# Performance work log

Measured on AMD Instinct MI355X. Metric: run time of the kernel, lower is better.

The kernel has to match this reference:

```python
import jax, jax.numpy as jnp
import numpy as np

DIM = 256
HID = int(DIM * 2.66)        # 680
CH = 2 * HID                 # 1360, TVConv channels
K = 3
K2 = K * K
HP, WP = 14, 14
POSI = 4
INTER = min(64, HID // 2)    # 64
EPS = 1e-5


def conv2d(x, w, pad):
    # x: (B, Cin, H, W), w: (Cout, Cin, kh, kw)
    return jax.lax.conv_general_dilated(
        x, w, window_strides=(1, 1), padding=[(pad, pad), (pad, pad)],
        dimension_numbers=("NCHW", "OIHW", "NCHW"))


def layernorm_chw(x, g, b):
    # torch nn.LayerNorm([C, H, W]): normalize over last 3 dims, affine (C,H,W)
    mu = jnp.mean(x, axis=(1, 2, 3), keepdims=True)
    var = jnp.var(x, axis=(1, 2, 3), keepdims=True)
    return (x - mu) * jax.lax.rsqrt(var + EPS) * g + b


def weight_layers(posi_map, w0, g0, b0, w1, g1, b1, w2, g2, b2, wf):
    h = jax.nn.relu(layernorm_chw(conv2d(posi_map, w0, 1), g0, b0))
    h = jax.nn.relu(layernorm_chw(conv2d(h, w1, 1), g1, b1))
    h = jax.nn.relu(layernorm_chw(conv2d(h, w2, 1), g2, b2))
    return conv2d(h, wf, 1)  # (1, CH*K2, HP, WP)


def tvconv(x, weight):
    # x: (B, CH, HP, WP); weight: (1, CH, K2, HP, WP)
    B, C, H, W = x.shape
    xp = jnp.pad(x, ((0, 0), (0, 0), (1, 1), (1, 1)))
    # unfold ordering: channel-major, kernel positions row-major -> axis=2
    patches = jnp.stack([xp[:, :, i:i + H, j:j + W]
                         for i in range(K) for j in range(K)], axis=2)
    return jnp.sum(weight * patches, axis=2)  # (B, CH, H, W)


def frfn_forward(x, W_in, posi_map, w0, g0, b0, w1, g1, b1, w2, g2, b2, wf, W_out):
    h = jnp.einsum('oc,bchw->bohw', W_in, x)                      # project_in (1x1)
    wgt = weight_layers(posi_map, w0, g0, b0, w1, g1, b1, w2, g2, b2, wf)
    wgt = wgt.reshape(1, CH, K2, HP, WP)
    h = tvconv(h, wgt)                                            # (B, CH, H, W)
    x1, x2 = h[:, :HID], h[:, HID:]
    h = jax.nn.gelu(x1, approximate=False) * x2
    return jnp.einsum('oc,bchw->bohw', W_out, h)                  # project_out (1x1)


def setup_inputs() -> dict:
    key = jax.random.key(0)
    ks = jax.random.split(key, 16)
    s = 0.02
    out_chans = CH * K2
    return {
        "x": jax.random.normal(ks[0], (64, DIM, HP, WP), jnp.float32),
        "W_in": jax.random.normal(ks[1], (CH, DIM), jnp.float32) * s,
        "posi_map": jnp.ones((1, POSI, HP, WP), jnp.float32),
        "w0": jax.random.normal(ks[2], (INTER, POSI, K, K), jnp.float32) * s,
        "g0": jnp.ones((INTER, HP, WP), jnp.float32),
        "b0": jnp.zeros((INTER, HP, WP), jnp.float32),
        "w1": jax.random.normal(ks[3], (INTER, INTER, K, K), jnp.float32) * s,
        "g1": jnp.ones((INTER, HP, WP), jnp.float32),
        "b1": jnp.zeros((INTER, HP, WP), jnp.float32),
        "w2": jax.random.normal(ks[4], (INTER, INTER, K, K), jnp.float32) * s,
        "g2": jnp.ones((INTER, HP, WP), jnp.float32),
        "b2": jnp.zeros((INTER, HP, WP), jnp.float32),
        "wf": jax.random.normal(ks[5], (out_chans, INTER, K, K), jnp.float32) * s,
        "W_out": jax.random.normal(ks[6], (DIM, HID), jnp.float32) * s,
    }


def reference(x, W_in, posi_map, w0, g0, b0, w1, g1, b1, w2, g2, b2, wf, W_out):
    return frfn_forward(x, W_in, posi_map, w0, g0, b0, w1, g1, b1, w2, g2, b2, wf, W_out)
```

## Files before the change

kernel.cpp:

```cpp
#include <hip/hip_runtime.h>
#include <math.h>

#define DIMC   256
#define HID    680
#define CHN    1360
#define HP     14
#define WP     14
#define P      196
#define POSI   4
#define INTER  64
#define BATCH  64
#define KPAD   704
#define OUTCH  12240
#define MW     1408
#define MTOT   12672
#define KIM    576
#define MPADIN 1408
#define EPSLN  1e-5f

typedef __attribute__((ext_vector_type(8))) short short8;
typedef __attribute__((ext_vector_type(4))) short short4v;
typedef __attribute__((ext_vector_type(4))) float f32x4;

#define OFS_WBIN  0u
#define OFS_WBOUT 720896u
#define OFS_XT    1081344u
#define OFS_V0    7503872u
#define OFS_V1    7554048u
#define OFS_V2    7604224u
#define OFS_WGTT  7654656u
#define OFS_H1T   12452736u
#define OFS_HGT   46580608u
#define OFS_IMC   64242560u
#define OFS_WFB   64468352u
#define OFS_PST   79066496u

__device__ __forceinline__ unsigned short f2bf(float f) {
    union { float f; unsigned u; } v; v.f = f;
    unsigned u = v.u;
    return (unsigned short)((u + 0x7FFFu + ((u >> 16) & 1u)) >> 16);
}
__device__ __forceinline__ float bf2f(unsigned short h) {
    union { unsigned u; float f; } v; v.u = ((unsigned)h) << 16; return v.f;
}

__device__ __forceinline__ void gl2lds16(const unsigned short* g, unsigned short* l) {
    __builtin_amdgcn_global_load_lds(
        (const __attribute__((address_space(1))) unsigned int*)g,
        (__attribute__((address_space(3))) unsigned int*)l, 16, 0, 0);
}
__device__ __forceinline__ short8 fragld64(const unsigned short* S, int row, int lp) {
    int slot = ((row >> 1) + lp) & 7;
    return *(const short8*)(S + row * 64 + slot * 8);
}

__device__ __forceinline__ void block_reduce2(float& s, float& ss, float* red, int tid, int nthreads) {
    #pragma unroll
    for (int off = 32; off > 0; off >>= 1) {
        s  += __shfl_down(s, off);
        ss += __shfl_down(ss, off);
    }
    int wid = tid >> 6, nw = nthreads >> 6;
    if ((tid & 63) == 0) { red[wid*2] = s; red[wid*2+1] = ss; }
    __syncthreads();
    if (tid == 0) {
        float S = 0.f, SS = 0.f;
        for (int i = 0; i < nw; i++) { S += red[i*2]; SS += red[i*2+1]; }
        red[0] = S; red[1] = SS;
    }
    __syncthreads();
    s = red[0]; ss = red[1];
}

__device__ __forceinline__ void sum_pstat(const float* __restrict__ pstat, int base,
                                          float& s, float& ss) {
    s = 0.f; ss = 0.f;
    #pragma unroll
    for (int i = 0; i < 49; i++) {
        s  += pstat[base + 2*i];
        ss += pstat[base + 2*i + 1];
    }
}

#define NWIN  (MPADIN*DIMC)
#define NWOUT (DIMC*KPAD)
#define XT0   49
#define WF0   561
#define C0    2343
#define IMZ0  2475
#define PRE_BLKS 2489

__global__ __launch_bounds__(256) void k_pre(const float* __restrict__ Win,
                                             const float* __restrict__ Wout,
                                             const float* __restrict__ x,
                                             const float* __restrict__ wf,
                                             const float* __restrict__ posi,
                                             const float* __restrict__ w0,
                                             unsigned short* __restrict__ Wbin,
                                             unsigned short* __restrict__ Wbout,
                                             unsigned short* __restrict__ Xt,
                                             unsigned short* __restrict__ wfb,
                                             unsigned short* __restrict__ imc,
                                             float* __restrict__ v0,
                                             float* __restrict__ pstat) {
    __shared__ __align__(16) float smem[6304];
    int bid = blockIdx.x, tid = threadIdx.x;
    if (bid < XT0) {
        float (*ppad)[16][16] = (float(*)[16][16])smem;
        float* red = smem + 1024;
        for (int i = tid; i < POSI * 256; i += 256) {
            int cc = i >> 8, r = i & 255, ly = r >> 4, lx = r & 15;
            float v = 0.f;
            if (ly >= 1 && ly <= HP && lx >= 1 && lx <= WP) v = posi[cc*P + (ly-1)*WP + (lx-1)];
            ppad[cc][ly][lx] = v;
        }
        __syncthreads();
        int gid = bid * 256 + tid;
        int c = gid / P, p = gid - c*P, y = p / WP, x2 = p - (p/WP)*WP;
        float v = 0.f;
        #pragma unroll
        for (int ci = 0; ci < POSI; ci++) {
            const float* wr = w0 + (c*POSI + ci)*9;
            v += wr[0]*ppad[ci][y  ][x2] + wr[1]*ppad[ci][y  ][x2+1] + wr[2]*ppad[ci][y  ][x2+2]
               + wr[3]*ppad[ci][y+1][x2] + wr[4]*ppad[ci][y+1][x2+1] + wr[5]*ppad[ci][y+1][x2+2]
               + wr[6]*ppad[ci][y+2][x2] + wr[7]*ppad[ci][y+2][x2+1] + wr[8]*ppad[ci][y+2][x2+2];
        }
        v0[gid] = v;
        float s = v, ss = v * v;
        block_reduce2(s, ss, red, tid, 256);
        if (tid == 0) { pstat[2*bid] = s; pstat[2*bid + 1] = ss; }
    } else if (bid < WF0) {
        int b2 = bid - XT0;
        int b = b2 >> 3, c0 = (b2 & 7) * 32;
        float* xs = smem;
        for (int i = tid; i < 32 * 49; i += 256) {
            int ci = i / 49, p4 = (i - ci * 49) * 4;
            float4 v = *(const float4*)(x + ((size_t)b * DIMC + c0 + ci) * P + p4);
            float* d = xs + ci * 197 + p4;
            d[0] = v.x; d[1] = v.y; d[2] = v.z; d[3] = v.w;
        }
        __syncthreads();
        for (int j = tid; j < P * 4; j += 256) {
            int pp = j >> 2, c8 = (j & 3) * 8;
            short8 o;
            #pragma unroll
            for (int e = 0; e < 8; e++) o[e] = (short)f2bf(xs[(c8 + e) * 197 + pp]);
            *(short8*)(Xt + ((size_t)b * P + pp) * DIMC + c0 + c8) = o;
        }
    } else if (bid < C0) {
        int base = (bid - WF0) * 1024;
        #pragma unroll
        for (int k2 = 0; k2 < 4; k2++) {
            int t = base + k2 * 256 + tid;
            int j = t * 4;
            int rowi = j / KIM, q = j - rowi * KIM;
            int kk = rowi / MW, ch = rowi - kk * MW;
            short4v sv = (short4v)0;
            if (ch < CHN) {
                float4 v = *(const float4*)(wf + ((size_t)(ch * 9 + kk)) * KIM + q);
                sv[0] = (short)f2bf(v.x); sv[1] = (short)f2bf(v.y);
                sv[2] = (short)f2bf(v.z); sv[3] = (short)f2bf(v.w);
            }
            *(short4v*)(wfb + j) = sv;
        }
    } else if (bid < IMZ0) {
        int base = (bid - C0) * 1024;
        #pragma unroll
        for (int k2 = 0; k2 < 4; k2++) {
            int t = base + k2 * 256 + tid;
            int i0 = t * 4;
            if (i0 < NWIN) {
                short4v sv = (short4v)0;
                if (i0 < CHN * DIMC) {
                    float4 v = *(const float4*)(Win + i0);
                    sv[0] = (short)f2bf(v.x); sv[1] = (short)f2bf(v.y);
                    sv[2] = (short)f2bf(v.z); sv[3] = (short)f2bf(v.w);
                }
                *(short4v*)(Wbin + i0) = sv;
            } else {
                int j0 = i0 - NWIN;
                int o = j0 / KPAD, k = j0 - o * KPAD;
                short4v sv = (short4v)0;
                if (k < HID) {
                    float4 v = *(const float4*)(Wout + o * HID + k);
                    sv[0] = (short)f2bf(v.x); sv[1] = (short)f2bf(v.y);
                    sv[2] = (short)f2bf(v.z); sv[3] = (short)f2bf(v.w);
                }
                *(short4v*)(Wbout + j0) = sv;
            }
        }
    } else {
        int base = (bid - IMZ0) * 1024;
        #pragma unroll
        for (int k2 = 0; k2 < 4; k2++) {
            int cc = base + k2 * 256 + tid;
            if (cc < (P * KIM) / 8) *(short8*)(imc + cc * 8) = (short8)0;
        }
    }
}


__device__ __forceinline__ void dev_convln(char* sm, int bid, int tid,
                                           const float* __restrict__ v_in,
                                           const float* __restrict__ g,
                                           const float* __restrict__ b,
                                           const float* __restrict__ w,
                                           float* __restrict__ v_out,
                                           float* __restrict__ pstat,
                                           int psi, int pso) {
    float* asf = (float*)sm;
    float* wlf = asf + INTER * 256;
    float* red = wlf + 3 * INTER * 12;
    const float inv = 1.f / (float)(INTER * P);
    float s0, ss0;
    sum_pstat(pstat, psi, s0, ss0);
    float mu = s0 * inv;
    float var = ss0 * inv - mu * mu;
    float rstd = rsqrtf(var + EPSLN);

    int gid0 = bid * 256;
    int cA = gid0 / P;
    for (int i = tid; i < 3 * INTER * 9; i += 512) {
        int cc = i / (INTER * 9), rest = i - cc * (INTER * 9);
        int ci = rest / 9, kk = rest - ci * 9;
        int crow = cA + cc; if (crow >= INTER) crow = INTER - 1;
        wlf[cc * (INTER * 12) + ci * 12 + kk] = w[(crow * INTER + ci) * 9 + kk];
    }
    for (int i = tid; i < INTER * 64; i += 512)
        *(f32x4*)(asf + i * 4) = (f32x4)0.f;
    __syncthreads();
    #pragma unroll
    for (int it = 0; it < 7; it++) {
        int q4 = it * 512 + tid;
        if (q4 < (INTER * P) / 4) {
            float4 vv = *(const float4*)(v_in + q4 * 4);
            float4 gg = *(const float4*)(g + q4 * 4);
            float4 bb = *(const float4*)(b + q4 * 4);
            float va[4] = {vv.x, vv.y, vv.z, vv.w};
            float ga[4] = {gg.x, gg.y, gg.z, gg.w};
            float ba[4] = {bb.x, bb.y, bb.z, bb.w};
            #pragma unroll
            for (int e = 0; e < 4; e++) {
                int idx = q4 * 4 + e;
                int ci = idx / P, p = idx - ci * P;
                int yy = p / WP, xx = p - yy * WP;
                float a = (va[e] - mu) * rstd * ga[e] + ba[e];
                asf[ci * 256 + (yy + 1) * 16 + (xx + 1)] = a > 0.f ? a : 0.f;
            }
        }
    }
    __syncthreads();
    float s = 0.f, ss = 0.f;
    if (tid < 256) {
        int gid = gid0 + tid;
        int c = gid / P, p = gid - c * P, y = p / WP, x = p - (p / WP) * WP;
        const float* wr0 = wlf + (c - cA) * (INTER * 12);
        float v = 0.f;
        for (int ci = 0; ci < INTER; ci++) {
            const float* wi = wr0 + ci * 12;
            const float* a0 = asf + ci * 256 + y * 16 + x;
            v += wi[0]*a0[0]  + wi[1]*a0[1]  + wi[2]*a0[2]
               + wi[3]*a0[16] + wi[4]*a0[17] + wi[5]*a0[18]
               + wi[6]*a0[32] + wi[7]*a0[33] + wi[8]*a0[34];
        }
        v_out[gid] = v;
        s = v; ss = v * v;
    }
    block_reduce2(s, ss, red, tid, 512);
    if (tid == 0) { pstat[pso + 2*bid] = s; pstat[pso + 2*bid + 1] = ss; }
}

__device__ __forceinline__ void dev_lnsc(int bid, int tid,
                                         const float* __restrict__ v_in,
                                         const float* __restrict__ g,
                                         const float* __restrict__ b,
                                         const float* __restrict__ pstat,
                                         unsigned short* __restrict__ imc) {
    if (tid >= 256) return;
    const float inv = 1.f / (float)(INTER * P);
    int gid = bid * 256 + tid;
    float s0, ss0;
    sum_pstat(pstat, 196, s0, ss0);
    float mu = s0 * inv;
    float var = ss0 * inv - mu * mu;
    float rstd = rsqrtf(var + EPSLN);
    float a = (v_in[gid] - mu) * rstd * g[gid] + b[gid];
    a = a > 0.f ? a : 0.f;
    unsigned short bv = f2bf(a);
    int ci = gid / P, p = gid - ci * P, y = p / WP, x = p - (p / WP) * WP;
    #pragma unroll
    for (int k = 0; k < 9; k++) {
        int yp = y - (k / 3 - 1), xp = x - (k % 3 - 1);
        if (yp >= 0 && yp < HP && xp >= 0 && xp < WP)
            imc[(yp * WP + xp) * KIM + ci * 9 + k] = bv;
    }
}

#define GIN_MT 11
#define GIN_NT 49
#define GIN_BLKS (GIN_MT * GIN_NT)
__device__ __forceinline__ void dev_gemm_in(char* sm, int mb, int nb, int tid,
                                            const unsigned short* __restrict__ A,
                                            const unsigned short* __restrict__ B,
                                            unsigned short* __restrict__ C) {
    unsigned short* As = (unsigned short*)sm;
    unsigned short* Bs = As + 128 * 64;
    int w = tid >> 6, lane = tid & 63, quad = lane >> 4, c16 = lane & 15;
    int m0 = mb * 128, n0 = nb * 256;
    int wm = (w & 1) * 64, wn = (w >> 1) * 64;
    f32x4 acc[4][4];
    #pragma unroll
    for (int i = 0; i < 4; i++)
        #pragma unroll
        for (int j = 0; j < 4; j++) acc[i][j] = (f32x4)0.f;

    for (int kc = 0; kc < 4; ++kc) {
        int k0 = kc * 64;
        if (kc) __syncthreads();
        #pragma unroll
        for (int i = tid; i < 1024; i += 512) {
            int r = i >> 3, s = i & 7, q = (s - (r >> 1)) & 7;
            gl2lds16(A + (size_t)(m0 + r) * DIMC + k0 + q * 8, As + (i & ~63) * 8);
        }
        #pragma unroll
        for (int i = tid; i < 2048; i += 512) {
            int r = i >> 3, s = i & 7, q = (s - (r >> 1)) & 7;
            gl2lds16(B + (size_t)(n0 + r) * DIMC + k0 + q * 8, Bs + (i & ~63) * 8);
        }
        __syncthreads();
        #pragma unroll
        for (int ks = 0; ks < 2; ++ks) {
            short8 af[4], bfr[4];
            #pragma unroll
            for (int i = 0; i < 4; i++) af[i] = fragld64(As, wm + i * 16 + c16, ks * 4 + quad);
            #pragma unroll
            for (int j = 0; j < 4; j++) bfr[j] = fragld64(Bs, wn + j * 16 + c16, ks * 4 + quad);
            #pragma unroll
            for (int i = 0; i < 4; i++)
                #pragma unroll
                for (int j = 0; j < 4; j++)
                    acc[i][j] = __builtin_amdgcn_mfma_f32_16x16x32_bf16(af[i], bfr[j], acc[i][j], 0, 0, 0);
        }
    }
    #pragma unroll
    for (int j = 0; j < 4; j++) {
        int n = n0 + wn + j * 16 + c16;
        unsigned short* dst = C + (size_t)n * CHN;
        #pragma unroll
        for (int i = 0; i < 4; i++) {
            int m = m0 + wm + i * 16 + quad * 4;
            if (m < CHN) {
                short4v sv;
                sv[0] = (short)f2bf(acc[i][j][0]);
                sv[1] = (short)f2bf(acc[i][j][1]);
                sv[2] = (short)f2bf(acc[i][j][2]);
                sv[3] = (short)f2bf(acc[i][j][3]);
                *(short4v*)(dst + m) = sv;
            }
        }
    }
}

__device__ __forceinline__ void dev_gemm_wf(char* sm, int bid, int tid,
                                            const unsigned short* __restrict__ wfb,
                                            const unsigned short* __restrict__ imc,
                                            unsigned short* __restrict__ wgtT) {
    unsigned short* buf = (unsigned short*)sm;
    unsigned short* As = buf;
    unsigned short* Bs = buf + 64 * 64;
    unsigned short* ot = buf;
    int w = tid >> 6, lane = tid & 63, quad = lane >> 4, c16 = lane & 15;
    int wq = w & 3;
    int f0 = (w < 4) ? 0 : 7;
    int fN = (w < 4) ? 7 : 6;
    int m0 = bid * 64;
    int kk = m0 / MW, ch0 = m0 - kk * MW;
    for (int i = tid; i < 96; i += 512)
        *(short8*)(Bs + 196 * 64 + i * 8) = (short8)0;
    f32x4 acc[7];
    #pragma unroll
    for (int f = 0; f < 7; f++) acc[f] = (f32x4)0.f;

    for (int kc = 0; kc < 9; ++kc) {
        int k0 = kc * 64;
        if (kc) __syncthreads();
        {
            int i = tid;
            int r = i >> 3, s = i & 7, q = (s - (r >> 1)) & 7;
            gl2lds16(wfb + ((size_t)(kk * MW + ch0 + r)) * KIM + k0 + q * 8, As + (i & ~63) * 8);
        }
        for (int i = tid; i < 1568; i += 512) {
            int r = i >> 3, s = i & 7, q = (s - (r >> 1)) & 7;
            gl2lds16(imc + (size_t)r * KIM + k0 + q * 8, Bs + (i & ~63) * 8);
        }
        __syncthreads();
        #pragma unroll
        for (int ks = 0; ks < 2; ++ks) {
            short8 af = fragld64(As, wq * 16 + c16, ks * 4 + quad);
            #pragma unroll
            for (int f = 0; f < 7; f++) {
                if (f < fN) {
                    short8 bf = fragld64(Bs, (f0 + f) * 16 + c16, ks * 4 + quad);
                    acc[f] = __builtin_amdgcn_mfma_f32_16x16x32_bf16(af, bf, acc[f], 0, 0, 0);
                }
            }
        }
    }
    __syncthreads();
    #pragma unroll
    for (int f = 0; f < 7; f++) {
        if (f < fN) {
            int p = (f0 + f) * 16 + c16;
            if (p < P) {
                short4v sv;
                sv[0] = (short)f2bf(acc[f][0]);
                sv[1] = (short)f2bf(acc[f][1]);
                sv[2] = (short)f2bf(acc[f][2]);
                sv[3] = (short)f2bf(acc[f][3]);
                *(short4v*)(ot + p * 72 + wq * 16 + quad * 4) = sv;
            }
        }
    }
    __syncthreads();
    int nvalid = CHN - ch0; if (nvalid > 64) nvalid = 64;
    for (int p = tid; p < P; p += 512) {
        const short8* src = (const short8*)(ot + p * 72);
        unsigned short* dst = wgtT + ((size_t)p * 9 + kk) * CHN + ch0;
        #pragma unroll
        for (int j = 0; j < 8; j++)
            if (j * 8 < nvalid) *(short8*)(dst + j * 8) = src[j];
    }
}

#define FA 0
#define FB 161
#define FC 321
#define FD 481
#define CONVLN_LDS ((INTER*256 + 3*INTER*12 + 16) * 4)
#define GIN_LDS    ((128*64 + 256*64) * 2)

extern __shared__ char dynsm[];

__global__ __launch_bounds__(512) void k_mA(const float* v0, const float* g0,
                                            const float* b0, const float* w1,
                                            float* v1, float* pstat,
                                            const unsigned short* Wbin,
                                            const unsigned short* Xt,
                                            unsigned short* h1t) {
    int bid = blockIdx.x, tid = threadIdx.x;
    if (bid < 49) dev_convln(dynsm, bid, tid, v0, g0, b0, w1, v1, pstat, 0, 98);
    else { int fid = FA + bid - 49; dev_gemm_in(dynsm, fid % GIN_MT, fid / GIN_MT, tid, Wbin, Xt, h1t); }
}
__global__ __launch_bounds__(512) void k_mB(const float* v1, const float* g1,
                                            const float* b1, const float* w2,
                                            float* v2, float* pstat,
                                            const unsigned short* Wbin,
                                            const unsigned short* Xt,
                                            unsigned short* h1t) {
    int bid = blockIdx.x, tid = threadIdx.x;
    if (bid < 49) dev_convln(dynsm, bid, tid, v1, g1, b1, w2, v2, pstat, 98, 196);
    else { int fid = FB + bid - 49; dev_gemm_in(dynsm, fid % GIN_MT, fid / GIN_MT, tid, Wbin, Xt, h1t); }
}
__global__ __launch_bounds__(512) void k_mC(const float* v2, const float* g2,
                                            const float* b2, const float* pstat,
                                            unsigned short* imc,
                                            const unsigned short* Wbin,
                                            const unsigned short* Xt,
                                            unsigned short* h1t) {
    int bid = blockIdx.x, tid = threadIdx.x;
    if (bid < 49) dev_lnsc(bid, tid, v2, g2, b2, pstat, imc);
    else { int fid = FC + bid - 49; dev_gemm_in(dynsm, fid % GIN_MT, fid / GIN_MT, tid, Wbin, Xt, h1t); }
}
__global__ __launch_bounds__(512) void k_mD(const unsigned short* wfb,
                                            const unsigned short* imc,
                                            unsigned short* wgtT,
                                            const unsigned short* Wbin,
                                            const unsigned short* Xt,
                                            unsigned short* h1t) {
    int bid = blockIdx.x, tid = threadIdx.x;
    if (bid < 198) dev_gemm_wf(dynsm, bid, tid, wfb, imc, wgtT);
    else { int fid = FD + bid - 198; dev_gemm_in(dynsm, fid % GIN_MT, fid / GIN_MT, tid, Wbin, Xt, h1t); }
}

__global__ __launch_bounds__(512) void k_tvg(const unsigned short* __restrict__ h1t,
                                             const unsigned short* __restrict__ wgtT,
                                             unsigned short* __restrict__ hgt) {
    __shared__ __align__(16) unsigned short wl[9 * CHN];
    int id = blockIdx.x;
    int xcd = id & 7, q = id >> 3;
    int p = xcd * 25 + (q % 25);
    int bg = q / 25;
    if (p >= P) return;
    int b0 = bg * 16, tid = threadIdx.x;
    const unsigned short* wrow = wgtT + (size_t)p * 9 * CHN;
    for (int i = tid * 8; i < 9 * CHN; i += 512 * 8)
        *(short8*)(wl + i) = *(const short8*)(wrow + i);
    int y = p / WP, x = p - (p / WP) * WP;
    int pn[9]; bool pv[9];
    #pragma unroll
    for (int k = 0; k < 9; k++) {
        int yy = y + k / 3 - 1, xx = x + (k % 3) - 1;
        pv[k] = (yy >= 0 && yy < HP && xx >= 0 && xx < WP);
        pn[k] = pv[k] ? yy * WP + xx : 0;
    }
    __syncthreads();
    for (int j = tid; j < 16 * 85; j += 512) {
        int bl = j / 85, c = (j - bl * 85) * 8;
        int b = b0 + bl;
        const unsigned short* hb = h1t + (size_t)b * P * CHN;
        float s1[8], s2[8];
        #pragma unroll
        for (int e = 0; e < 8; e++) { s1[e] = 0.f; s2[e] = 0.f; }
        #pragma unroll
        for (int k = 0; k < 9; k++) {
            if (!pv[k]) continue;
            const unsigned short* hr = hb + (size_t)pn[k] * CHN + c;
            short8 h1v = *(const short8*)hr;
            short8 h2v = *(const short8*)(hr + HID);
            short8 w1v = *(const short8*)(wl + k * CHN + c);
            short8 w2v = *(const short8*)(wl + k * CHN + HID + c);
            #pragma unroll
            for (int e = 0; e < 8; e++) {
                s1[e] += bf2f((unsigned short)w1v[e]) * bf2f((unsigned short)h1v[e]);
                s2[e] += bf2f((unsigned short)w2v[e]) * bf2f((unsigned short)h2v[e]);
            }
        }
        short8 o;
        #pragma unroll
        for (int e = 0; e < 8; e++) {
            float gl = 0.5f * s1[e] * (1.f + erff(s1[e] * 0.70710678118654752f));
            o[e] = (short)f2bf(gl * s2[e]);
        }
        *(short8*)(hgt + ((size_t)b * P + p) * KPAD + c) = o;
    }
    if (tid < 48) {
        int bl = tid / 3, z = (tid - bl * 3) * 8;
        *(short8*)(hgt + ((size_t)(b0 + bl) * P + p) * KPAD + HID + z) = (short8)0;
    }
}

__global__ __launch_bounds__(256) void k_gemm_out(const unsigned short* __restrict__ A,
                                                  const unsigned short* __restrict__ B,
                                                  float* __restrict__ out) {
    __shared__ __align__(16) unsigned short As[64 * 64];
    __shared__ __align__(16) unsigned short Bs[128 * 64];
    int tid = threadIdx.x;
    int w = tid >> 6, lane = tid & 63, quad = lane >> 4, c16 = lane & 15;
    int m0 = blockIdx.x * 64, n0 = blockIdx.y * 128;
    int wm = (w & 1) * 32, wn = (w >> 1) * 64;
    f32x4 acc[2][4];
    #pragma unroll
    for (int i = 0; i < 2; i++)
        #pragma unroll
        for (int j = 0; j < 4; j++) acc[i][j] = (f32x4)0.f;

    for (int kc = 0; kc < 11; ++kc) {
        int k0 = kc * 64;
        if (kc) __syncthreads();
        #pragma unroll
        for (int i = tid; i < 512; i += 256) {
            int r = i >> 3, s = i & 7, q = (s - (r >> 1)) & 7;
            gl2lds16(A + (size_t)(m0 + r) * KPAD + k0 + q * 8, As + (i & ~63) * 8);
        }
        #pragma unroll
        for (int i = tid; i < 1024; i += 256) {
            int r = i >> 3, s = i & 7, q = (s - (r >> 1)) & 7;
            gl2lds16(B + (size_t)(n0 + r) * KPAD + k0 + q * 8, Bs + (i & ~63) * 8);
        }
        __syncthreads();
        #pragma unroll
        for (int ks = 0; ks < 2; ++ks) {
            short8 af[2], bfr[4];
            #pragma unroll
            for (int i = 0; i < 2; i++) af[i] = fragld64(As, wm + i * 16 + c16, ks * 4 + quad);
            #pragma unroll
            for (int j = 0; j < 4; j++) bfr[j] = fragld64(Bs, wn + j * 16 + c16, ks * 4 + quad);
            #pragma unroll
            for (int i = 0; i < 2; i++)
                #pragma unroll
                for (int j = 0; j < 4; j++)
                    acc[i][j] = __builtin_amdgcn_mfma_f32_16x16x32_bf16(af[i], bfr[j], acc[i][j], 0, 0, 0);
        }
    }
    #pragma unroll
    for (int j = 0; j < 4; j++) {
        int n = n0 + wn + j * 16 + c16;
        int b = n / P, pp = n - b * P;
        #pragma unroll
        for (int i = 0; i < 2; i++) {
            int m = m0 + wm + i * 16 + quad * 4;
            #pragma unroll
            for (int r = 0; r < 4; r++)
                out[((size_t)b * DIMC + m + r) * P + pp] = acc[i][j][r];
        }
    }
}

extern "C" void kernel_launch(void* const* d_in, const int* in_sizes, int n_in,
                              void* d_out, int out_size, void* d_ws, size_t ws_size,
                              hipStream_t stream) {
    (void)in_sizes; (void)n_in; (void)out_size; (void)ws_size;
    const float* x     = (const float*)d_in[0];
    const float* W_in  = (const float*)d_in[1];
    const float* posi  = (const float*)d_in[2];
    const float* w0    = (const float*)d_in[3];
    const float* g0    = (const float*)d_in[4];
    const float* b0    = (const float*)d_in[5];
    const float* w1    = (const float*)d_in[6];
    const float* g1    = (const float*)d_in[7];
    const float* b1    = (const float*)d_in[8];
    const float* w2    = (const float*)d_in[9];
    const float* g2    = (const float*)d_in[10];
    const float* b2    = (const float*)d_in[11];
    const float* wf    = (const float*)d_in[12];
    const float* W_out = (const float*)d_in[13];
    float* out = (float*)d_out;
    char* ws = (char*)d_ws;

    unsigned short* Wbin  = (unsigned short*)(ws + OFS_WBIN);
    unsigned short* Wbout = (unsigned short*)(ws + OFS_WBOUT);
    unsigned short* Xt    = (unsigned short*)(ws + OFS_XT);
    float*          v0    = (float*)(ws + OFS_V0);
    float*          v1    = (float*)(ws + OFS_V1);
    float*          v2    = (float*)(ws + OFS_V2);
    float*          pstat = (float*)(ws + OFS_PST);
    unsigned short* wgtT  = (unsigned short*)(ws + OFS_WGTT);
    unsigned short* h1t   = (unsigned short*)(ws + OFS_H1T);
    unsigned short* hgt   = (unsigned short*)(ws + OFS_HGT);
    unsigned short* imc   = (unsigned short*)(ws + OFS_IMC);
    unsigned short* wfb   = (unsigned short*)(ws + OFS_WFB);

    k_pre<<<PRE_BLKS, 256, 0, stream>>>(
        W_in, W_out, x, wf, posi, w0, Wbin, Wbout, Xt, wfb, imc, v0, pstat);
    k_mA<<<49 + (FB - FA), 512, CONVLN_LDS, stream>>>(v0, g0, b0, w1, v1, pstat, Wbin, Xt, h1t);
    k_mB<<<49 + (FC - FB), 512, CONVLN_LDS, stream>>>(v1, g1, b1, w2, v2, pstat, Wbin, Xt, h1t);
    k_mC<<<49 + (FD - FC), 512, CONVLN_LDS, stream>>>(v2, g2, b2, pstat, imc, Wbin, Xt, h1t);
    k_mD<<<198 + (GIN_BLKS - FD), 512, GIN_LDS, stream>>>(wfb, imc, wgtT, Wbin, Xt, h1t);
    k_tvg     <<<800, 512, 0, stream>>>(h1t, wgtT, hgt);
    k_gemm_out<<<dim3(DIMC/64, (BATCH*P)/128), 256, 0, stream>>>(Wbout, hgt, out);
}
```

Measured before the change: 211.8 us.

## Fuse TVConv-GELU stage with output projection GEMM per pixel

Merges the TVConv+GELU-gating kernel and the project_out GEMM into one kernel. Each block handles one pixel and 32 batch items, computes the gated hidden activations in 128-channel chunks into LDS, and immediately runs MFMA against W_out rows read directly from global memory. This removes the hgt intermediate round trip and one kernel launch. In exchange, W_out is re-read by every block, the per-pixel GEMM tile is small (256x32), and output stores are strided across pixels.

New measurement: 232.9 us. 9.9% more time.

```diff
diff --git a/kernel.cpp b/kernel.cpp
--- a/kernel.cpp
+++ b/kernel.cpp
@@ -30,7 +30,6 @@
 #define OFS_V2    7604224u
 #define OFS_WGTT  7654656u
 #define OFS_H1T   12452736u
-#define OFS_HGT   46580608u
 #define OFS_IMC   64242560u
 #define OFS_WFB   64468352u
 #define OFS_PST   79066496u
@@ -482,16 +481,21 @@
     else { int fid = FD + bid - 198; dev_gemm_in(dynsm, fid % GIN_MT, fid / GIN_MT, tid, Wbin, Xt, h1t); }
 }
 
-__global__ __launch_bounds__(512) void k_tvg(const unsigned short* __restrict__ h1t,
-                                             const unsigned short* __restrict__ wgtT,
-                                             unsigned short* __restrict__ hgt) {
+__global__ __launch_bounds__(512) void k_tvgo(const unsigned short* __restrict__ h1t,
+                                              const unsigned short* __restrict__ wgtT,
+                                              const unsigned short* __restrict__ Wbout,
+                                              float* __restrict__ out) {
     __shared__ __align__(16) unsigned short wl[9 * CHN];
+    __shared__ __align__(16) unsigned short hgbuf[2][32 * 64];
     int id = blockIdx.x;
     int xcd = id & 7, q = id >> 3;
     int p = xcd * 25 + (q % 25);
     int bg = q / 25;
     if (p >= P) return;
-    int b0 = bg * 16, tid = threadIdx.x;
+    int b0 = bg * 32, tid = threadIdx.x;
+    int w = tid >> 6, lane = tid & 63, quad = lane >> 4, c16 = lane & 15;
+    int wm = w * 32;
+
     const unsigned short* wrow = wgtT + (size_t)p * 9 * CHN;
     for (int i = tid * 8; i < 9 * CHN; i += 512 * 8)
         *(short8*)(wl + i) = *(const short8*)(wrow + i);
@@ -503,95 +507,80 @@
         pv[k] = (yy >= 0 && yy < HP && xx >= 0 && xx < WP);
         pn[k] = pv[k] ? yy * WP + xx : 0;
     }
-    __syncthreads();
-    for (int j = tid; j < 16 * 85; j += 512) {
-        int bl = j / 85, c = (j - bl * 85) * 8;
-        int b = b0 + bl;
-        const unsigned short* hb = h1t + (size_t)b * P * CHN;
-        float s1[8], s2[8];
-        #pragma unroll
-        for (int e = 0; e < 8; e++) { s1[e] = 0.f; s2[e] = 0.f; }
-        #pragma unroll
-        for (int k = 0; k < 9; k++) {
-            if (!pv[k]) continue;
-            const unsigned short* hr = hb + (size_t)pn[k] * CHN + c;
-            short8 h1v = *(const short8*)hr;
-            short8 h2v = *(const short8*)(hr + HID);
-            short8 w1v = *(const short8*)(wl + k * CHN + c);
-            short8 w2v = *(const short8*)(wl + k * CHN + HID + c);
-            #pragma unroll
-            for (int e = 0; e < 8; e++) {
-                s1[e] += bf2f((unsigned short)w1v[e]) * bf2f((unsigned short)h1v[e]);
-                s2[e] += bf2f((unsigned short)w2v[e]) * bf2f((unsigned short)h2v[e]);
-            }
-        }
-        short8 o;
-        #pragma unroll
-        for (int e = 0; e < 8; e++) {
-            float gl = 0.5f * s1[e] * (1.f + erff(s1[e] * 0.70710678118654752f));
-            o[e] = (short)f2bf(gl * s2[e]);
-        }
-        *(short8*)(hgt + ((size_t)b * P + p) * KPAD + c) = o;
-    }
-    if (tid < 48) {
-        int bl = tid / 3, z = (tid - bl * 3) * 8;
-        *(short8*)(hgt + ((size_t)(b0 + bl) * P + p) * KPAD + HID + z) = (short8)0;
-    }
-}
-
-__global__ __launch_bounds__(256) void k_gemm_out(const unsigned short* __restrict__ A,
-                                                  const unsigned short* __restrict__ B,
-                                                  float* __restrict__ out) {
-    __shared__ __align__(16) unsigned short As[64 * 64];
-    __shared__ __align__(16) unsigned short Bs[128 * 64];
-    int tid = threadIdx.x;
-    int w = tid >> 6, lane = tid & 63, quad = lane >> 4, c16 = lane & 15;
-    int m0 = blockIdx.x * 64, n0 = blockIdx.y * 128;
-    int wm = (w & 1) * 32, wn = (w >> 1) * 64;
-    f32x4 acc[2][4];
+    int bl = tid >> 4, g = tid & 15;
+    int gs = g >> 3, glp = g & 7;
+    unsigned short* hdst = hgbuf[gs] + bl * 64 + (((bl >> 1) + glp) & 7) * 8;
+    const unsigned short* hb = h1t + (size_t)(b0 + bl) * P * CHN;
+
+    f32x4 acc[2][2];
     #pragma unroll
     for (int i = 0; i < 2; i++)
         #pragma unroll
-        for (int j = 0; j < 4; j++) acc[i][j] = (f32x4)0.f;
-
-    for (int kc = 0; kc < 11; ++kc) {
-        int k0 = kc * 64;
-        if (kc) __syncthreads();
-        #pragma unroll
-        for (int i = tid; i < 512; i += 256) {
-            int r = i >> 3, s = i & 7, q = (s - (r >> 1)) & 7;
-            gl2lds16(A + (size_t)(m0 + r) * KPAD + k0 + q * 8, As + (i & ~63) * 8);
-        }
-        #pragma unroll
-        for (int i = tid; i < 1024; i += 256) {
-            int r = i >> 3, s = i & 7, q = (s - (r >> 1)) & 7;
-            gl2lds16(B + (size_t)(n0 + r) * KPAD + k0 + q * 8, Bs + (i & ~63) * 8);
+        for (int j = 0; j < 2; j++) acc[i][j] = (f32x4)0.f;
+
+    for (int cc = 0; cc < 6; ++cc) {
+        int c0 = cc * 128;
+        if (cc) __syncthreads();
+        {
+            int c = c0 + g * 8;
+            short8 o = (short8)0;
+            if (c < HID) {
+                float s1[8], s2[8];
+                #pragma unroll
+                for (int e = 0; e < 8; e++) { s1[e] = 0.f; s2[e] = 0.f; }
+                #pragma unroll
+                for (int k = 0; k < 9; k++) {
+                    if (!pv[k]) continue;
+                    const unsigned short* hr = hb + (size_t)pn[k] * CHN + c;
+                    short8 h1v = *(const short8*)hr;
+                    short8 h2v = *(const short8*)(hr + HID);
+                    short8 w1v = *(const short8*)(wl + k * CHN + c);
+                    short8 w2v = *(const short8*)(wl + k * CHN + HID + c);
+                    #pragma unroll
+                    for (int e = 0; e < 8; e++) {
+                        s1[e] += bf2f((unsigned short)w1v[e]) * bf2f((unsigned short)h1v[e]);
+                        s2[e] += bf2f((unsigned short)w2v[e]) * bf2f((unsigned short)h2v[e]);
+                    }
+                }
+                #pragma unroll
+                for (int e = 0; e < 8; e++) {
+                    float gl = 0.5f * s1[e] * (1.f + erff(s1[e] * 0.70710678118654752f));
+                    o[e] = (short)f2bf(gl * s2[e]);
+                }
+            }
+            *(short8*)hdst = o;
         }
         __syncthreads();
-        #pragma unroll
-        for (int ks = 0; ks < 2; ++ks) {
-            short8 af[2], bfr[4];
-            #pragma unroll
-            for (int i = 0; i < 2; i++) af[i] = fragld64(As, wm + i * 16 + c16, ks * 4 + quad);
-            #pragma unroll
-            for (int j = 0; j < 4; j++) bfr[j] = fragld64(Bs, wn + j * 16 + c16, ks * 4 + quad);
-            #pragma unroll
-            for (int i = 0; i < 2; i++)
+        int nsub = (cc < 5) ? 2 : 1;
+        for (int s = 0; s < nsub; ++s) {
+            int kbase = c0 + s * 64;
+            #pragma unroll
+            for (int ks = 0; ks < 2; ++ks) {
+                short8 af[2], bfr[2];
                 #pragma unroll
-                for (int j = 0; j < 4; j++)
-                    acc[i][j] = __builtin_amdgcn_mfma_f32_16x16x32_bf16(af[i], bfr[j], acc[i][j], 0, 0, 0);
-        }
-    }
-    #pragma unroll
-    for (int j = 0; j < 4; j++) {
-        int n = n0 + wn + j * 16 + c16;
-        int b = n / P, pp = n - b * P;
+                for (int i = 0; i < 2; i++)
+                    af[i] = *(const short8*)(Wbout + (size_t)(wm + i * 16 + c16) * KPAD
+                                             + kbase + (ks * 4 + quad) * 8);
+                #pragma unroll
+                for (int j = 0; j < 2; j++)
+                    bfr[j] = fragld64(hgbuf[s], j * 16 + c16, ks * 4 + quad);
+                #pragma unroll
+                for (int i = 0; i < 2; i++)
+                    #pragma unroll
+                    for (int j = 0; j < 2; j++)
+                        acc[i][j] = __builtin_amdgcn_mfma_f32_16x16x32_bf16(af[i], bfr[j], acc[i][j], 0, 0, 0);
+            }
+        }
+    }
+    #pragma unroll
+    for (int j = 0; j < 2; j++) {
+        int b = b0 + j * 16 + c16;
         #pragma unroll
         for (int i = 0; i < 2; i++) {
-            int m = m0 + wm + i * 16 + quad * 4;
+            int m = wm + i * 16 + quad * 4;
             #pragma unroll
             for (int r = 0; r < 4; r++)
-                out[((size_t)b * DIMC + m + r) * P + pp] = acc[i][j][r];
+                out[((size_t)b * DIMC + m + r) * P + p] = acc[i][j][r];
         }
     }
 }
@@ -626,7 +615,6 @@
     float*          pstat = (float*)(ws + OFS_PST);
     unsigned short* wgtT  = (unsigned short*)(ws + OFS_WGTT);
     unsigned short* h1t   = (unsigned short*)(ws + OFS_H1T);
-    unsigned short* hgt   = (unsigned short*)(ws + OFS_HGT);
     unsigned short* imc   = (unsigned short*)(ws + OFS_IMC);
     unsigned short* wfb   = (unsigned short*)(ws + OFS_WFB);
 
@@ -636,6 +624,5 @@
     k_mB<<<49 + (FC - FB), 512, CONVLN_LDS, stream>>>(v1, g1, b1, w2, v2, pstat, Wbin, Xt, h1t);
     k_mC<<<49 + (FD - FC), 512, CONVLN_LDS, stream>>>(v2, g2, b2, pstat, imc, Wbin, Xt, h1t);
     k_mD<<<198 + (GIN_BLKS - FD), 512, GIN_LDS, stream>>>(wfb, imc, wgtT, Wbin, Xt, h1t);
-    k_tvg     <<<800, 512, 0, stream>>>(h1t, wgtT, hgt);
-    k_gemm_out<<<dim3(DIMC/64, (BATCH*P)/128), 256, 0, stream>>>(Wbout, hgt, out);
-}
+    k_tvgo<<<400, 512, 0, stream>>>(h1t, wgtT, Wbout, out);
+}
```
